# Kernel tuning notes

Measured on AMD Instinct MI355X. Metric: run time of the kernel, lower is better.

Reference implementation:

```python
import jax, jax.numpy as jnp
import numpy as np

# Layer sizes: (input_dim, hidden_dim) matching nn.LSTM(1,300),(300,256),(256,64),(64,1)
_SIZES = [(1, 300), (300, 256), (256, 64), (64, 1)]


def setup_inputs() -> dict:
    key = jax.random.key(0)
    ks = jax.random.split(key, 17)
    B, T = 128, 1024
    inp = {"x": jax.random.normal(ks[0], (B, T, 1), dtype=jnp.float32)}
    i = 1
    for l, (din, h) in enumerate(_SIZES, start=1):
        s = 1.0 / np.sqrt(h)  # PyTorch LSTM default init: U(-1/sqrt(H), 1/sqrt(H))
        inp[f"w_ih{l}"] = jax.random.uniform(ks[i], (4 * h, din), jnp.float32, -s, s); i += 1
        inp[f"w_hh{l}"] = jax.random.uniform(ks[i], (4 * h, h), jnp.float32, -s, s); i += 1
        inp[f"b_ih{l}"] = jax.random.uniform(ks[i], (4 * h,), jnp.float32, -s, s); i += 1
        inp[f"b_hh{l}"] = jax.random.uniform(ks[i], (4 * h,), jnp.float32, -s, s); i += 1
    return inp


def _lstm_layer(x, w_ih, w_hh, b_ih, b_hh):
    """Single-layer batch_first LSTM, zero initial state. x: [B,T,Din] -> [B,T,H]."""
    B, T, _ = x.shape
    H = w_hh.shape[1]
    # Precompute input projection for all timesteps at once: [B,T,4H]
    xp = jnp.einsum('bti,gi->btg', x, w_ih) + b_ih + b_hh

    def step(carry, xt):
        h, c = carry
        gates = xt + h @ w_hh.T  # [B,4H]
        i_g, f_g, g_g, o_g = jnp.split(gates, 4, axis=-1)  # PyTorch gate order i,f,g,o
        c = jax.nn.sigmoid(f_g) * c + jax.nn.sigmoid(i_g) * jnp.tanh(g_g)
        h = jax.nn.sigmoid(o_g) * jnp.tanh(c)
        return (h, c), h

    h0 = jnp.zeros((B, H), x.dtype)
    (_, _), ys = jax.lax.scan(step, (h0, h0), jnp.swapaxes(xp, 0, 1))  # ys: [T,B,H]
    return jnp.swapaxes(ys, 0, 1)


def reference(x, w_ih1, w_hh1, b_ih1, b_hh1,
              w_ih2, w_hh2, b_ih2, b_hh2,
              w_ih3, w_hh3, b_ih3, b_hh3,
              w_ih4, w_hh4, b_ih4, b_hh4):
    # Note: dropout=0.3 in the torch module is a no-op (num_layers=1 per LSTM).
    x = _lstm_layer(x, w_ih1, w_hh1, b_ih1, b_hh1)
    x = _lstm_layer(x, w_ih2, w_hh2, b_ih2, b_hh2)
    x = _lstm_layer(x, w_ih3, w_hh3, b_ih3, b_hh3)
    x = _lstm_layer(x, w_ih4, w_hh4, b_ih4, b_hh4)
    return x[:, -1, :]  # [B, 1]
```

## Files before the change

kernel.cpp:

```cpp
#include <hip/hip_runtime.h>

#define B 128
#define T 1024

typedef unsigned short u16;
typedef unsigned int   u32;
typedef unsigned long long u64;

__device__ __forceinline__ float sigm(float x){ return 1.f/(1.f+__expf(-x)); }
__device__ __forceinline__ float tanh_(float x){ return 1.f - 2.f/(1.f+__expf(2.f*x)); }
__device__ __forceinline__ u16 f2b(float f){
  u32 u = __float_as_uint(f);
  u += 0x7FFFu + ((u>>16)&1u);
  return (u16)(u>>16);
}
__device__ __forceinline__ float bf(u16 s){ return __uint_as_float(((u32)s)<<16); }
__device__ __forceinline__ float blo(u32 q){ return __uint_as_float(q<<16); }
__device__ __forceinline__ float bhi(u32 q){ return __uint_as_float(q & 0xffff0000u); }

__device__ __align__(16) u64 g_h1T[(u32)16*T*304*2];
__device__ __align__(16) u64 g_h2T[(u32)16*T*256*2];
__device__ u16    g_xp3[(u32)B*T*256];
__device__ float4 g_xp4[(u32)B*T];
__device__ int    g_cnt[2][16][32];

__global__ void k_zero_flags(){
  int i = threadIdx.x;
  if (i < 2*16*32) ((int*)g_cnt)[i] = 0;
}

__global__ __launch_bounds__(320) void k_l1(const float* __restrict__ x,
    const float* __restrict__ wih, const float* __restrict__ whh,
    const float* __restrict__ bih, const float* __restrict__ bhh){
  __shared__ float sW[304*84];
  __shared__ uint4 sV[304];
  __shared__ float sG[80*8];
  __shared__ float sBsum[80], sWih[80];
  __shared__ float sXall[8*1024];
  const int tid = threadIdx.x;
  const int cl = blockIdx.x / 15, wg = blockIdx.x % 15;
  const int b0 = cl*8, u0 = wg*20;

  for (int idx = tid; idx < 304*20; idx += 320){
    int k = idx / 20, c = idx % 20;
    int rq = c + 20 - (k & 15); if (rq >= 20) rq -= 20;
    float4 w;
    #pragma unroll
    for (int j = 0; j < 4; ++j){
      int r = 4*rq + j;
      int g = r / 20, ul = r % 20;
      int grow = g*300 + u0 + ul;
      (&w.x)[j] = (k < 300) ? whh[grow*300 + k] : 0.f;
    }
    *(float4*)&sW[k*84 + 4*c] = w;
  }
  for (int idx = tid; idx < 80; idx += 320){
    int g = idx / 20, ul = idx % 20;
    int grow = g*300 + u0 + ul;
    sBsum[idx] = bih[grow] + bhh[grow];
    sWih[idx]  = wih[grow];
  }
  for (int idx = tid; idx < 8*1024; idx += 320){
    int b = idx >> 10, t = idx & 1023;
    sXall[t*8 + b] = x[(b0+b)*1024 + t];
  }
  if (tid < 304) sV[tid] = make_uint4(0,0,0,0);
  __syncthreads();

  const int rq = tid >> 4, ks = tid & 15;
  int cq = rq + ks; if (cq >= 20) cq -= 20;
  float c_state = 0.f;
  int* cnt = &g_cnt[0][cl][0];

  for (int t = 0; t < T; ++t){
    float acc[4][8];
    #pragma unroll
    for (int j=0;j<4;++j){
      #pragma unroll
      for (int b=0;b<8;++b) acc[j][b] = 0.f;
    }
    #pragma unroll 4
    for (int kk = 0; kk < 19; ++kk){
      int k = kk*16 + ks;
      float4 w = *(const float4*)&sW[k*84 + 4*cq];
      uint4 q = sV[k];
      float v[8] = { blo(q.x), bhi(q.x), blo(q.y), bhi(q.y),
                     blo(q.z), bhi(q.z), blo(q.w), bhi(q.w) };
      #pragma unroll
      for (int j=0;j<4;++j){
        float wj = (&w.x)[j];
        #pragma unroll
        for (int b=0;b<8;++b) acc[j][b] = __builtin_fmaf(wj, v[b], acc[j][b]);
      }
    }
    #pragma unroll
    for (int m = 1; m < 16; m <<= 1){
      #pragma unroll
      for (int j=0;j<4;++j){
        #pragma unroll
        for (int b=0;b<8;++b) acc[j][b] += __shfl_xor(acc[j][b], m);
      }
    }
    if (ks < 8){
      int j = ks >> 1, h = ks & 1;
      *(float4*)&sG[(4*rq + j)*8 + 4*h] =
        make_float4(acc[j][4*h+0], acc[j][4*h+1], acc[j][4*h+2], acc[j][4*h+3]);
    }
    __syncthreads();
    if (tid < 160){
      int u = tid >> 3, b = tid & 7;
      float gs[4];
      #pragma unroll
      for (int g=0; g<4; ++g){
        int r = g*20 + u;
        gs[g] = sBsum[r] + sXall[t*8+b]*sWih[r] + sG[r*8 + b];
      }
      float cg = sigm(gs[1])*c_state + sigm(gs[0])*tanh_(gs[2]);
      c_state = cg;
      float h = sigm(gs[3])*tanh_(cg);
      u32 us = f2b(h);
      u32 other = (u32)__shfl_xor((int)us, 1);
      if (!(b & 1)){
        u32 pk = us | (other << 16);
        u32 widx = ((u32)(cl*T + t)*304 + (u32)(u0 + u))*4 + (u32)(b >> 1);
        __hip_atomic_store((u32*)g_h1T + widx, pk, __ATOMIC_RELAXED, __HIP_MEMORY_SCOPE_AGENT);
      }
    }
    __syncthreads();
    if (tid == 0)
      __hip_atomic_fetch_add(cnt, 1, __ATOMIC_RELAXED, __HIP_MEMORY_SCOPE_AGENT);
    if (t+1 < T){
      if (tid == 0){
        while (__hip_atomic_load(cnt, __ATOMIC_RELAXED, __HIP_MEMORY_SCOPE_AGENT) < (t+1)*15) {}
      }
      __syncthreads();
      if (tid < 300){
        u32 base = ((u32)(cl*T + t)*304 + (u32)tid)*2;
        u64 lo = __hip_atomic_load(&g_h1T[base],   __ATOMIC_RELAXED, __HIP_MEMORY_SCOPE_AGENT);
        u64 hi = __hip_atomic_load(&g_h1T[base+1], __ATOMIC_RELAXED, __HIP_MEMORY_SCOPE_AGENT);
        sV[tid] = make_uint4((u32)lo, (u32)(lo>>32), (u32)hi, (u32)(hi>>32));
      }
      __syncthreads();
    }
  }
}

__global__ __launch_bounds__(256) void k_l2(
    const float* __restrict__ wih, const float* __restrict__ whh,
    const float* __restrict__ bih, const float* __restrict__ bhh){
  __shared__ float sWr[256*72];
  __shared__ u16   sWx[304*72];
  __shared__ uint4 sVh[256];
  __shared__ uint4 sVx[2][304];
  __shared__ float sG[64*8];
  __shared__ float sBsum[64];
  const int tid = threadIdx.x;
  const int cl = blockIdx.x >> 4, wg = blockIdx.x & 15;
  const int u0 = wg*16;

  for (int idx = tid; idx < 256*16; idx += 256){
    int k = idx >> 4, c = idx & 15;
    int rqs = c ^ (k & 15);
    float4 w;
    #pragma unroll
    for (int j=0;j<4;++j){
      int r = 4*rqs + j; int g = r >> 4, ul = r & 15;
      (&w.x)[j] = whh[(g*256 + u0 + ul)*256 + k];
    }
    *(float4*)&sWr[k*72 + 4*c] = w;
  }
  for (int idx = tid; idx < 304*16; idx += 256){
    int k = idx >> 4, c = idx & 15;
    int rqs = c ^ (k & 15);
    ushort4 w;
    #pragma unroll
    for (int j=0;j<4;++j){
      int r = 4*rqs + j; int g = r >> 4, ul = r & 15;
      float wv = (k < 300) ? wih[(g*256 + u0 + ul)*300 + k] : 0.f;
      (&w.x)[j] = f2b(wv);
    }
    *(ushort4*)&sWx[k*72 + 4*c] = w;
  }
  for (int idx = tid; idx < 64; idx += 256){
    int g = idx >> 4, ul = idx & 15;
    int grow = g*256 + u0 + ul;
    sBsum[idx] = bih[grow] + bhh[grow];
  }
  sVh[tid] = make_uint4(0,0,0,0);
  for (int kx = tid; kx < 304; kx += 256)
    sVx[0][kx] = *(const uint4*)&g_h1T[((u32)(cl*T + 0)*304 + (u32)kx)*2];
  __syncthreads();

  const int rq = tid >> 4, ks = tid & 15;
  const int cq = rq ^ ks;
  float c_state = 0.f;
  int* cnt = &g_cnt[1][cl][0];
  int cur = 0;

  for (int t = 0; t < T; ++t){
    uint4 pf0 = make_uint4(0,0,0,0), pf1 = pf0;
    if (t+1 < T && tid < 152){
      u32 base = ((u32)(cl*T + (t+1))*304)*2;
      pf0 = *(const uint4*)&g_h1T[base + (u32)tid*2];
      pf1 = *(const uint4*)&g_h1T[base + (u32)(tid+152)*2];
    }
    float acc[4][8];
    #pragma unroll
    for (int j=0;j<4;++j){
      #pragma unroll
      for (int b=0;b<8;++b) acc[j][b] = 0.f;
    }
    #pragma unroll 4
    for (int kk = 0; kk < 19; ++kk){
      int k = kk*16 + ks;
      ushort4 wu = *(const ushort4*)&sWx[k*72 + 4*cq];
      uint4 q = sVx[cur][k];
      float v[8] = { blo(q.x), bhi(q.x), blo(q.y), bhi(q.y),
                     blo(q.z), bhi(q.z), blo(q.w), bhi(q.w) };
      #pragma unroll
      for (int j=0;j<4;++j){
        float wj = bf((&wu.x)[j]);
        #pragma unroll
        for (int b=0;b<8;++b) acc[j][b] = __builtin_fmaf(wj, v[b], acc[j][b]);
      }
    }
    #pragma unroll 4
    for (int kk = 0; kk < 16; ++kk){
      int k = kk*16 + ks;
      float4 w = *(const float4*)&sWr[k*72 + 4*cq];
      uint4 q = sVh[k];
      float v[8] = { blo(q.x), bhi(q.x), blo(q.y), bhi(q.y),
                     blo(q.z), bhi(q.z), blo(q.w), bhi(q.w) };
      #pragma unroll
      for (int j=0;j<4;++j){
        float wj = (&w.x)[j];
        #pragma unroll
        for (int b=0;b<8;++b) acc[j][b] = __builtin_fmaf(wj, v[b], acc[j][b]);
      }
    }
    #pragma unroll
    for (int m = 1; m < 16; m <<= 1){
      #pragma unroll
      for (int j=0;j<4;++j){
        #pragma unroll
        for (int b=0;b<8;++b) acc[j][b] += __shfl_xor(acc[j][b], m);
      }
    }
    if (ks < 8){
      int j = ks >> 1, h = ks & 1;
      *(float4*)&sG[(4*rq + j)*8 + 4*h] =
        make_float4(acc[j][4*h+0], acc[j][4*h+1], acc[j][4*h+2], acc[j][4*h+3]);
    }
    __syncthreads();
    if (tid < 128){
      int u = tid >> 3, b = tid & 7;
      float gs[4];
      #pragma unroll
      for (int g=0; g<4; ++g){
        int r = g*16 + u;
        gs[g] = sBsum[r] + sG[r*8 + b];
      }
      float cg = sigm(gs[1])*c_state + sigm(gs[0])*tanh_(gs[2]);
      c_state = cg;
      float h = sigm(gs[3])*tanh_(cg);
      u32 us = f2b(h);
      u32 other = (u32)__shfl_xor((int)us, 1);
      if (!(b & 1)){
        u32 pk = us | (other << 16);
        u32 widx = ((u32)(cl*T + t)*256 + (u32)(u0 + u))*4 + (u32)(b >> 1);
        __hip_atomic_store((u32*)g_h2T + widx, pk, __ATOMIC_RELAXED, __HIP_MEMORY_SCOPE_AGENT);
      }
    }
    __syncthreads();
    if (tid == 0)
      __hip_atomic_fetch_add(cnt, 1, __ATOMIC_RELAXED, __HIP_MEMORY_SCOPE_AGENT);
    if (t+1 < T){
      if (tid < 152){ sVx[cur^1][tid] = pf0; sVx[cur^1][tid+152] = pf1; }
      if (tid == 0){
        while (__hip_atomic_load(cnt, __ATOMIC_RELAXED, __HIP_MEMORY_SCOPE_AGENT) < (t+1)*16) {}
      }
      __syncthreads();
      {
        u32 base = ((u32)(cl*T + t)*256 + (u32)tid)*2;
        u64 lo = __hip_atomic_load(&g_h2T[base],   __ATOMIC_RELAXED, __HIP_MEMORY_SCOPE_AGENT);
        u64 hi = __hip_atomic_load(&g_h2T[base+1], __ATOMIC_RELAXED, __HIP_MEMORY_SCOPE_AGENT);
        sVh[tid] = make_uint4((u32)lo, (u32)(lo>>32), (u32)hi, (u32)(hi>>32));
      }
      __syncthreads();
      cur ^= 1;
    }
  }
}

__global__ __launch_bounds__(256) void k_g3(const float* __restrict__ wih3){
  __shared__ u16 At[256*72];
  __shared__ u16 Bt[256*72];
  const int tid = threadIdx.x;
  const int nt = blockIdx.x & 3, mt = blockIdx.x >> 2;
  const int cl = mt >> 7, t0 = (mt & 127)*8, n0 = nt*64;
  {
    int i = tid >> 5, kb = tid & 31;
    for (int kk = 0; kk < 8; ++kk){
      int k = kk*32 + kb;
      uint4 q = *(const uint4*)&g_h2T[((u32)(cl*T + t0 + i)*256 + (u32)k)*2];
      *(uint4*)&At[k*72 + i*8] = q;
    }
  }
  {
    int nl = tid & 63, kq4 = tid >> 6;
    for (int kk = 0; kk < 16; ++kk){
      int kq = kq4*16 + kk;
      float4 w = *(const float4*)&wih3[(n0+nl)*256 + 4*kq];
      #pragma unroll
      for (int m=0;m<4;++m) Bt[(4*kq+m)*72 + nl] = f2b((&w.x)[m]);
    }
  }
  __syncthreads();
  const int r4 = tid >> 4, c4 = tid & 15;
  float acc[4][4];
  #pragma unroll
  for (int j=0;j<4;++j){
    #pragma unroll
    for (int m=0;m<4;++m) acc[j][m] = 0.f;
  }
  #pragma unroll 4
  for (int k = 0; k < 256; ++k){
    ushort4 a = *(const ushort4*)&At[k*72 + 4*r4];
    ushort4 b = *(const ushort4*)&Bt[k*72 + 4*c4];
    float av[4] = { bf(a.x), bf(a.y), bf(a.z), bf(a.w) };
    float bv[4] = { bf(b.x), bf(b.y), bf(b.z), bf(b.w) };
    #pragma unroll
    for (int j=0;j<4;++j){
      #pragma unroll
      for (int m=0;m<4;++m) acc[j][m] = __builtin_fmaf(av[j], bv[m], acc[j][m]);
    }
  }
  #pragma unroll
  for (int j=0;j<4;++j){
    int l = 4*r4 + j;
    int tt = t0 + (l >> 3), bg = cl*8 + (l & 7);
    ushort4 o;
    #pragma unroll
    for (int m=0;m<4;++m) (&o.x)[m] = f2b(acc[j][m]);
    *(ushort4*)&g_xp3[((u32)bg*T + (u32)tt)*256 + (u32)(n0 + 4*c4)] = o;
  }
}

__global__ __launch_bounds__(64) void k_l3(
    const float* __restrict__ whh, const float* __restrict__ bih,
    const float* __restrict__ bhh, const float* __restrict__ wih4){
  __shared__ float sW[64*256];
  __shared__ float sV[64];
  __shared__ float sG[256];
  __shared__ float sBs[256];
  const int lane = threadIdx.x;
  const int b = blockIdx.x;
  #pragma unroll 1
  for (int j = 0; j < 4; ++j){
    int r = 4*lane + j;
    for (int kq = 0; kq < 16; ++kq){
      float4 w = *(const float4*)&whh[r*64 + 4*kq];
      #pragma unroll
      for (int m=0;m<4;++m) sW[(4*kq+m)*256 + r] = (&w.x)[m];
    }
  }
  for (int idx = lane; idx < 256; idx += 64) sBs[idx] = bih[idx] + bhh[idx];
  float w4g[4];
  #pragma unroll
  for (int g=0;g<4;++g) w4g[g] = wih4[g*64 + lane];
  sV[lane] = 0.f;
  float c_state = 0.f;
  __syncthreads();

  for (int t = 0; t < T; ++t){
    u16 xr[4];
    #pragma unroll
    for (int g=0;g<4;++g) xr[g] = g_xp3[((u32)b*T + (u32)t)*256 + (u32)(g*64 + lane)];
    float a0=0.f, a1=0.f, a2=0.f, a3=0.f;
    #pragma unroll 4
    for (int k4 = 0; k4 < 16; ++k4){
      float4 v4 = *(const float4*)&sV[4*k4];
      #pragma unroll
      for (int m=0;m<4;++m){
        float4 w = *(const float4*)&sW[(4*k4+m)*256 + 4*lane];
        float vm = (&v4.x)[m];
        a0 = __builtin_fmaf(w.x, vm, a0);
        a1 = __builtin_fmaf(w.y, vm, a1);
        a2 = __builtin_fmaf(w.z, vm, a2);
        a3 = __builtin_fmaf(w.w, vm, a3);
      }
    }
    *(float4*)&sG[4*lane] = make_float4(a0,a1,a2,a3);
    __syncthreads();
    float gs[4];
    #pragma unroll
    for (int g=0;g<4;++g) gs[g] = sBs[g*64 + lane] + bf(xr[g]) + sG[g*64 + lane];
    float cg = sigm(gs[1])*c_state + sigm(gs[0])*tanh_(gs[2]);
    c_state = cg;
    float h = sigm(gs[3])*tanh_(cg);
    sV[lane] = h;
    float p[4];
    #pragma unroll
    for (int g=0;g<4;++g) p[g] = w4g[g]*h;
    #pragma unroll
    for (int off = 32; off; off >>= 1){
      #pragma unroll
      for (int g=0;g<4;++g) p[g] += __shfl_down(p[g], off);
    }
    if (lane == 0) g_xp4[(u32)b*T + t] = make_float4(p[0],p[1],p[2],p[3]);
    __syncthreads();
  }
}

__global__ void k_l4(const float* __restrict__ whh, const float* __restrict__ bih,
                     const float* __restrict__ bhh, float* __restrict__ out){
  int b = blockIdx.x*64 + threadIdx.x;
  float wi=whh[0], wf=whh[1], wg=whh[2], wo=whh[3];
  float bi=bih[0]+bhh[0], bf_=bih[1]+bhh[1], bg=bih[2]+bhh[2], bo=bih[3]+bhh[3];
  float h=0.f, c=0.f;
  const float4* xp = &g_xp4[(u32)b*T];
  float4 nxt = xp[0];
  for (int t=0; t<T; ++t){
    float4 cur = nxt;
    if (t+1 < T) nxt = xp[t+1];
    float ig = sigm(cur.x + wi*h + bi);
    float fg = sigm(cur.y + wf*h + bf_);
    float gg = tanh_(cur.z + wg*h + bg);
    float og = sigm(cur.w + wo*h + bo);
    c = fg*c + ig*gg;
    h = og*tanh_(c);
  }
  out[b] = h;
}

extern "C" void kernel_launch(void* const* d_in, const int* in_sizes, int n_in,
                              void* d_out, int out_size, void* d_ws, size_t ws_size,
                              hipStream_t stream){
  (void)in_sizes; (void)n_in; (void)d_ws; (void)ws_size; (void)out_size;
  const float* x    = (const float*)d_in[0];
  const float* wih1 = (const float*)d_in[1];
  const float* whh1 = (const float*)d_in[2];
  const float* bih1 = (const float*)d_in[3];
  const float* bhh1 = (const float*)d_in[4];
  const float* wih2 = (const float*)d_in[5];
  const float* whh2 = (const float*)d_in[6];
  const float* bih2 = (const float*)d_in[7];
  const float* bhh2 = (const float*)d_in[8];
  const float* wih3 = (const float*)d_in[9];
  const float* whh3 = (const float*)d_in[10];
  const float* bih3 = (const float*)d_in[11];
  const float* bhh3 = (const float*)d_in[12];
  const float* wih4 = (const float*)d_in[13];
  const float* whh4 = (const float*)d_in[14];
  const float* bih4 = (const float*)d_in[15];
  const float* bhh4 = (const float*)d_in[16];

  hipLaunchKernelGGL(k_zero_flags, dim3(1), dim3(1024), 0, stream);
  hipLaunchKernelGGL(k_l1, dim3(240), dim3(320), 0, stream, x, wih1, whh1, bih1, bhh1);
  hipLaunchKernelGGL(k_l2, dim3(256), dim3(256), 0, stream, wih2, whh2, bih2, bhh2);
  hipLaunchKernelGGL(k_g3, dim3(8192), dim3(256), 0, stream, wih3);
  hipLaunchKernelGGL(k_l3, dim3(128), dim3(64), 0, stream, whh3, bih3, bhh3, wih4);
  hipLaunchKernelGGL(k_l4, dim3(2), dim3(64), 0, stream, whh4, bih4, bhh4, (float*)d_out);
}
```

Before: 13.57 ms.

## Replace shared atomic counters with per-block flags and overlap L2 wait with input matvec

Each workgroup now publishes its completed timestep to its own padded flag slot instead of atomically incrementing a shared counter, and several threads poll the flags in parallel. In layer 2, the wait for the previous step's hidden state is moved after the input-projection matvec, so that independent work runs while peer blocks finish. This is meant to cut atomic contention and per-step barrier latency on the recurrent critical path. The cost is more polling traffic, a larger flag buffer to zero, and a more delicate cross-block ordering.

Measured after the change: 14.11 ms. +4.0%, slower.

```diff
diff --git a/kernel.cpp b/kernel.cpp
--- a/kernel.cpp
+++ b/kernel.cpp
@@ -22,11 +22,11 @@
 __device__ __align__(16) u64 g_h2T[(u32)16*T*256*2];
 __device__ u16    g_xp3[(u32)B*T*256];
 __device__ float4 g_xp4[(u32)B*T];
-__device__ int    g_cnt[2][16][32];
+__device__ int    g_flag[2][16][16*32];
 
 __global__ void k_zero_flags(){
-  int i = threadIdx.x;
-  if (i < 2*16*32) ((int*)g_cnt)[i] = 0;
+  int i = blockIdx.x*1024 + threadIdx.x;
+  if (i < 2*16*16*32) ((int*)g_flag)[i] = 0;
 }
 
 __global__ __launch_bounds__(320) void k_l1(const float* __restrict__ x,
@@ -70,7 +70,7 @@
   const int rq = tid >> 4, ks = tid & 15;
   int cq = rq + ks; if (cq >= 20) cq -= 20;
   float c_state = 0.f;
-  int* cnt = &g_cnt[0][cl][0];
+  int* flg = &g_flag[0][cl][0];
 
   for (int t = 0; t < T; ++t){
     float acc[4][8];
@@ -128,10 +128,11 @@
     }
     __syncthreads();
     if (tid == 0)
-      __hip_atomic_fetch_add(cnt, 1, __ATOMIC_RELAXED, __HIP_MEMORY_SCOPE_AGENT);
+      __hip_atomic_store(&flg[wg*32], t+1, __ATOMIC_RELAXED, __HIP_MEMORY_SCOPE_AGENT);
     if (t+1 < T){
-      if (tid == 0){
-        while (__hip_atomic_load(cnt, __ATOMIC_RELAXED, __HIP_MEMORY_SCOPE_AGENT) < (t+1)*15) {}
+      if (tid < 15){
+        const int* fp = &flg[tid*32];
+        while (__hip_atomic_load(fp, __ATOMIC_RELAXED, __HIP_MEMORY_SCOPE_AGENT) < t+1) {}
       }
       __syncthreads();
       if (tid < 300){
@@ -194,7 +195,7 @@
   const int rq = tid >> 4, ks = tid & 15;
   const int cq = rq ^ ks;
   float c_state = 0.f;
-  int* cnt = &g_cnt[1][cl][0];
+  int* flg = &g_flag[1][cl][0];
   int cur = 0;
 
   for (int t = 0; t < T; ++t){
@@ -223,6 +224,20 @@
         #pragma unroll
         for (int b=0;b<8;++b) acc[j][b] = __builtin_fmaf(wj, v[b], acc[j][b]);
       }
+    }
+    if (t > 0){
+      if (tid < 16){
+        const int* fp = &flg[tid*32];
+        while (__hip_atomic_load(fp, __ATOMIC_RELAXED, __HIP_MEMORY_SCOPE_AGENT) < t) {}
+      }
+      __syncthreads();
+      {
+        u32 base = ((u32)(cl*T + (t-1))*256 + (u32)tid)*2;
+        u64 lo = __hip_atomic_load(&g_h2T[base],   __ATOMIC_RELAXED, __HIP_MEMORY_SCOPE_AGENT);
+        u64 hi = __hip_atomic_load(&g_h2T[base+1], __ATOMIC_RELAXED, __HIP_MEMORY_SCOPE_AGENT);
+        sVh[tid] = make_uint4((u32)lo, (u32)(lo>>32), (u32)hi, (u32)(hi>>32));
+      }
+      __syncthreads();
     }
     #pragma unroll 4
     for (int kk = 0; kk < 16; ++kk){
@@ -271,24 +286,11 @@
         __hip_atomic_store((u32*)g_h2T + widx, pk, __ATOMIC_RELAXED, __HIP_MEMORY_SCOPE_AGENT);
       }
     }
-    __syncthreads();
-    if (tid == 0)
-      __hip_atomic_fetch_add(cnt, 1, __ATOMIC_RELAXED, __HIP_MEMORY_SCOPE_AGENT);
-    if (t+1 < T){
-      if (tid < 152){ sVx[cur^1][tid] = pf0; sVx[cur^1][tid+152] = pf1; }
-      if (tid == 0){
-        while (__hip_atomic_load(cnt, __ATOMIC_RELAXED, __HIP_MEMORY_SCOPE_AGENT) < (t+1)*16) {}
-      }
-      __syncthreads();
-      {
-        u32 base = ((u32)(cl*T + t)*256 + (u32)tid)*2;
-        u64 lo = __hip_atomic_load(&g_h2T[base],   __ATOMIC_RELAXED, __HIP_MEMORY_SCOPE_AGENT);
-        u64 hi = __hip_atomic_load(&g_h2T[base+1], __ATOMIC_RELAXED, __HIP_MEMORY_SCOPE_AGENT);
-        sVh[tid] = make_uint4((u32)lo, (u32)(lo>>32), (u32)hi, (u32)(hi>>32));
-      }
-      __syncthreads();
-      cur ^= 1;
-    }
+    if (t+1 < T && tid < 152){ sVx[cur^1][tid] = pf0; sVx[cur^1][tid+152] = pf1; }
+    __syncthreads();
+    if (tid == 0 && t+1 < T)
+      __hip_atomic_store(&flg[wg*32], t+1, __ATOMIC_RELAXED, __HIP_MEMORY_SCOPE_AGENT);
+    cur ^= 1;
   }
 }
 
@@ -455,7 +457,7 @@
   const float* bih4 = (const float*)d_in[15];
   const float* bhh4 = (const float*)d_in[16];
 
-  hipLaunchKernelGGL(k_zero_flags, dim3(1), dim3(1024), 0, stream);
+  hipLaunchKernelGGL(k_zero_flags, dim3(16), dim3(1024), 0, stream);
   hipLaunchKernelGGL(k_l1, dim3(240), dim3(320), 0, stream, x, wih1, whh1, bih1, bhh1);
   hipLaunchKernelGGL(k_l2, dim3(256), dim3(256), 0, stream, wih2, whh2, bih2, bhh2);
   hipLaunchKernelGGL(k_g3, dim3(8192), dim3(256), 0, stream, wih3);
```
